# Performance work log

Hardware: AMD Instinct MI355X
Metric: run time of the kernel (lower is better)

## Reference

```python
import jax, jax.numpy as jnp
import numpy as np

B = 16384          # scenes (batch_size)
K = 16             # vehicles per scene (1 hero + 15 neighbors)
IN_LEN = 16        # in_length
OUT_LEN = 25       # out_length
ALL_LEN = 41       # all_length
T_H = IN_LEN - 1
ENC = 64           # encoder_size
N = B * K
NN = B * (K - 1)


def setup_inputs() -> dict:
    key = jax.random.key(0)
    ks = jax.random.split(key, 20)
    scene = jax.random.normal(ks[0], (N, 2, ALL_LEN), jnp.float32)
    idx = jnp.arange(N, dtype=jnp.int32)
    hero_index = idx[::K]                 # hero is first vehicle of each group
    nbr_index = idx[idx % K != 0]         # remaining K-1 vehicles, group-major
    w = lambda k, s: jax.random.normal(k, s, jnp.float32) * 0.1
    return {
        'scene': scene, 'hero_index': hero_index, 'nbr_index': nbr_index,
        'W_h1': w(ks[1], (2 * IN_LEN, 32)), 'b_h1': w(ks[2], (32,)),
        'W_h2': w(ks[3], (32, ENC)), 'b_h2': w(ks[4], (ENC,)),
        'W_f1': w(ks[5], (2 * OUT_LEN, 32)), 'b_f1': w(ks[6], (32,)),
        'W_f2': w(ks[7], (32, ENC)), 'b_f2': w(ks[8], (ENC,)),
        'W_dyn': w(ks[9], (ENC, 32)), 'b_dyn': w(ks[10], (32,)),
        'W_nbr': w(ks[11], (2 * IN_LEN, ENC)), 'b_nbr': w(ks[12], (ENC,)),
        'W_out': w(ks[13], (96, 128)), 'b_out': w(ks[14], (128,)),
        'W_op': w(ks[15], (128, 1)), 'b_op': w(ks[16], (1,)),
    }


def reference(scene, hero_index, nbr_index,
              W_h1, b_h1, W_h2, b_h2, W_f1, b_f1, W_f2, b_f2,
              W_dyn, b_dyn, W_nbr, b_nbr, W_out, b_out, W_op, b_op):
    lrelu = lambda x: jax.nn.leaky_relu(x, 0.1)
    # per-scene reference pose = hero position at t_h, broadcast to all vehicles
    ref = scene[hero_index, :, T_H][:, :, None]              # (B,2,1)
    scene = scene - jnp.repeat(ref, K, axis=0)               # (N,2,ALL_LEN)
    # per-scene, per-channel scale = max |history| over vehicles and time
    scale = jnp.abs(scene[:, :, :IN_LEN]).reshape(B, K, 2, IN_LEN).max(axis=(1, 3))  # (B,2)
    scene = scene / jnp.repeat(scale, K, axis=0)[:, :, None]
    hero = scene[hero_index]                                 # (B,2,ALL_LEN)
    nbrs = scene[nbr_index]                                  # (NN,2,ALL_LEN)
    hist = hero[:, :, :IN_LEN].transpose(0, 2, 1)            # (B,IN_LEN,2)
    fut = hero[:, :, IN_LEN:IN_LEN + OUT_LEN].transpose(0, 2, 1)  # (B,OUT_LEN,2)
    nb_hist = nbrs[:, :, :IN_LEN].transpose(0, 2, 1)         # (NN,IN_LEN,2)
    rel = jnp.repeat(hist, K - 1, axis=0) - nb_hist          # (NN,IN_LEN,2)
    hist_f = hist.reshape(B, 2 * IN_LEN)
    fut_f = fut.reshape(B, 2 * OUT_LEN)
    rel_f = rel.reshape(NN, 2 * IN_LEN)
    # hero history encoder (mlp_net) + dyn_emb
    hist_enc = lrelu(lrelu(hist_f @ W_h1 + b_h1) @ W_h2 + b_h2)
    hist_enc = lrelu(hist_enc @ W_dyn + b_dyn)
    # neighbor relative encoder + per-scene max pool + dyn_emb
    rela_enc = lrelu(rel_f @ W_nbr + b_nbr)                  # (NN,ENC)
    pooled = rela_enc.reshape(B, K - 1, ENC).max(axis=1)     # (B,ENC)
    pooled = lrelu(pooled @ W_dyn + b_dyn)
    # future encoder (mlp_net_fut) + dyn_emb
    fut_enc = lrelu(lrelu(fut_f @ W_f1 + b_f1) @ W_f2 + b_f2)
    fut_enc = lrelu(fut_enc @ W_dyn + b_dyn)
    enc = jnp.concatenate([hist_enc, pooled, fut_enc], axis=1)  # (B,96)
    feature_enc = lrelu(enc @ W_out + b_out)                 # (B,128)
    logit = jax.nn.sigmoid(feature_enc @ W_op + b_op)        # (B,1)
    return logit, feature_enc
```

## Files before the change

kernel.cpp:

```cpp
#include <hip/hip_runtime.h>
#include <math.h>

#define NB 16384

typedef short short8 __attribute__((ext_vector_type(8)));
typedef float f32x4 __attribute__((ext_vector_type(4)));

__device__ __forceinline__ float lrelu(float x){ return x > 0.f ? x : 0.1f*x; }

__device__ __forceinline__ unsigned short f2b(float f){
  unsigned u = __builtin_bit_cast(unsigned, f);
  u = (u + 0x7fffu + ((u >> 16) & 1u)) >> 16;
  return (unsigned short)u;
}

__device__ __forceinline__ short8 afrag(const unsigned short* tile, int stride_us, int kbase){
  const int l = threadIdx.x & 63;
  return *(const short8*)(tile + (size_t)(l & 15) * stride_us + kbase + ((l >> 4) * 8));
}

__device__ __forceinline__ short8 wfragT(const float* __restrict__ W, int ldn,
                                         int nbase, int kbase, int K){
  const int l = threadIdx.x & 63;
  const int n = nbase + (l & 15);
  const int k0 = kbase + ((l >> 4) * 8);
  short8 r;
  #pragma unroll
  for (int e = 0; e < 8; ++e){
    const int k = k0 + e;
    const float v = (k < K) ? W[k * ldn + n] : 0.f;
    r[e] = (short)f2b(v);
  }
  return r;
}

#define MFMA(a,b,c) __builtin_amdgcn_mfma_f32_16x16x32_bf16((a),(b),(c),0,0,0)

__global__ __launch_bounds__(512) void highway_fused(
    const float* __restrict__ scene,
    const float* __restrict__ W_h1, const float* __restrict__ b_h1,
    const float* __restrict__ W_h2, const float* __restrict__ b_h2,
    const float* __restrict__ W_f1, const float* __restrict__ b_f1,
    const float* __restrict__ W_f2, const float* __restrict__ b_f2,
    const float* __restrict__ W_dyn, const float* __restrict__ b_dyn,
    const float* __restrict__ W_nbr, const float* __restrict__ b_nbr,
    const float* __restrict__ W_out, const float* __restrict__ b_out,
    const float* __restrict__ W_op, const float* __restrict__ b_op,
    float* __restrict__ logit, float* __restrict__ feat)
{
  __shared__ __align__(16) unsigned short An[15][16][40];
  __shared__ __align__(16) unsigned short Ah[16][40];
  __shared__ __align__(16) unsigned short Af[16][72];
  __shared__ __align__(16) unsigned short Apool[16][72];
  __shared__ __align__(16) unsigned short As1h[16][40];
  __shared__ __align__(16) unsigned short As1f[16][40];
  __shared__ __align__(16) unsigned short As2h[16][72];
  __shared__ __align__(16) unsigned short As2f[16][72];
  __shared__ __align__(16) unsigned short Aenc[16][104];
  __shared__ float tmpP[4][16][16];
  __shared__ float red[8][16];

  const int tid = threadIdx.x;
  const int w = tid >> 6, l = tid & 63;
  const int g = tid >> 5;
  const int s = tid & 31;
  const int c = s >> 4, t = s & 15;
  const int g0 = blockIdx.x * 16;
  const float* sc = scene + (size_t)(g0 + g) * 1312;

  const short8 wn  = wfragT(W_nbr, 64, (w & 3) * 16, 0, 32);
  const short8 s1a = (w < 2) ? wfragT(W_h1, 32, (w & 1) * 16, 0, 32)
                             : wfragT(W_f1, 32, (w & 1) * 16, 0, 50);
  const short8 s1b = wfragT(W_f1, 32, (w & 1) * 16, 32, 50);
  const short8 wd0 = wfragT(W_dyn, 32, (w & 1) * 16, 0, 64);
  const short8 wd1 = wfragT(W_dyn, 32, (w & 1) * 16, 32, 64);
  const short8 s2  = (w < 4) ? wfragT(W_h2, 64, w * 16, 0, 32)
                             : wfragT(W_f2, 64, (w & 3) * 16, 0, 32);
  const short8 wo0 = wfragT(W_out, 128, w * 16, 0, 96);
  const short8 wo1 = wfragT(W_out, 128, w * 16, 32, 96);
  const short8 wo2 = wfragT(W_out, 128, w * 16, 64, 96);
  const float  wop = W_op[w * 16 + (l & 15)];

  float v[16];
  #pragma unroll
  for (int k = 0; k < 16; ++k) v[k] = sc[k * 82 + c * 41 + t];
  const float vf0 = sc[c * 41 + 16 + t];
  const float vf1 = (t < 9) ? sc[c * 41 + 32 + t] : 0.f;

  const float ref = __shfl(v[0], (l & 32) | (c << 4) | 15, 64);
  float m = 0.f;
  #pragma unroll
  for (int k = 0; k < 16; ++k) m = fmaxf(m, fabsf(v[k] - ref));
  m = fmaxf(m, __shfl_xor(m, 1, 64));
  m = fmaxf(m, __shfl_xor(m, 2, 64));
  m = fmaxf(m, __shfl_xor(m, 4, 64));
  m = fmaxf(m, __shfl_xor(m, 8, 64));
  const float inv = 1.f / m;

  Ah[g][2 * t + c] = f2b((v[0] - ref) * inv);
  #pragma unroll
  for (int j = 0; j < 15; ++j)
    An[j][g][2 * t + c] = f2b((v[0] - v[j + 1]) * inv);
  Af[g][2 * t + c] = f2b((vf0 - ref) * inv);
  Af[g][2 * t + 32 + c] = (t < 9) ? f2b((vf1 - ref) * inv) : (unsigned short)0;

  __syncthreads();

  {
    const int nt = w & 3;
    const int jbase = (w >> 2) * 8;
    const int njt = (w >> 2) ? 7 : 8;
    const float bn = b_nbr[nt * 16 + (l & 15)];
    f32x4 pm = {-1e30f, -1e30f, -1e30f, -1e30f};
    for (int jj = 0; jj < njt; ++jj){
      const short8 a = afrag(&An[jbase + jj][0][0], 40, 0);
      f32x4 acc = {0.f, 0.f, 0.f, 0.f};
      acc = MFMA(a, wn, acc);
      #pragma unroll
      for (int r = 0; r < 4; ++r) pm[r] = fmaxf(pm[r], lrelu(acc[r] + bn));
    }
    if (w >= 4){
      #pragma unroll
      for (int r = 0; r < 4; ++r) tmpP[nt][(l >> 4) * 4 + r][l & 15] = pm[r];
    }
    __syncthreads();
    if (w < 4){
      #pragma unroll
      for (int r = 0; r < 4; ++r){
        const float q = fmaxf(pm[r], tmpP[nt][(l >> 4) * 4 + r][l & 15]);
        Apool[(l >> 4) * 4 + r][nt * 16 + (l & 15)] = f2b(q);
      }
    }
  }
  __syncthreads();

  if (w < 2){
    const short8 a = afrag(&Ah[0][0], 40, 0);
    f32x4 acc = {0.f, 0.f, 0.f, 0.f};
    acc = MFMA(a, s1a, acc);
    const float bb = b_h1[(w & 1) * 16 + (l & 15)];
    #pragma unroll
    for (int r = 0; r < 4; ++r)
      As1h[(l >> 4) * 4 + r][(w & 1) * 16 + (l & 15)] = f2b(lrelu(acc[r] + bb));
  } else if (w < 4){
    const short8 a0 = afrag(&Af[0][0], 72, 0);
    const short8 a1 = afrag(&Af[0][0], 72, 32);
    f32x4 acc = {0.f, 0.f, 0.f, 0.f};
    acc = MFMA(a0, s1a, acc);
    acc = MFMA(a1, s1b, acc);
    const float bb = b_f1[(w & 1) * 16 + (l & 15)];
    #pragma unroll
    for (int r = 0; r < 4; ++r)
      As1f[(l >> 4) * 4 + r][(w & 1) * 16 + (l & 15)] = f2b(lrelu(acc[r] + bb));
  } else if (w < 6){
    const short8 a0 = afrag(&Apool[0][0], 72, 0);
    const short8 a1 = afrag(&Apool[0][0], 72, 32);
    f32x4 acc = {0.f, 0.f, 0.f, 0.f};
    acc = MFMA(a0, wd0, acc);
    acc = MFMA(a1, wd1, acc);
    const float bb = b_dyn[(w & 1) * 16 + (l & 15)];
    #pragma unroll
    for (int r = 0; r < 4; ++r)
      Aenc[(l >> 4) * 4 + r][32 + (w & 1) * 16 + (l & 15)] = f2b(lrelu(acc[r] + bb));
  }
  __syncthreads();

  if (w < 4){
    const short8 a = afrag(&As1h[0][0], 40, 0);
    f32x4 acc = {0.f, 0.f, 0.f, 0.f};
    acc = MFMA(a, s2, acc);
    const float bb = b_h2[w * 16 + (l & 15)];
    #pragma unroll
    for (int r = 0; r < 4; ++r)
      As2h[(l >> 4) * 4 + r][w * 16 + (l & 15)] = f2b(lrelu(acc[r] + bb));
  } else {
    const short8 a = afrag(&As1f[0][0], 40, 0);
    f32x4 acc = {0.f, 0.f, 0.f, 0.f};
    acc = MFMA(a, s2, acc);
    const float bb = b_f2[(w & 3) * 16 + (l & 15)];
    #pragma unroll
    for (int r = 0; r < 4; ++r)
      As2f[(l >> 4) * 4 + r][(w & 3) * 16 + (l & 15)] = f2b(lrelu(acc[r] + bb));
  }
  __syncthreads();

  if (w < 2){
    const short8 a0 = afrag(&As2h[0][0], 72, 0);
    const short8 a1 = afrag(&As2h[0][0], 72, 32);
    f32x4 acc = {0.f, 0.f, 0.f, 0.f};
    acc = MFMA(a0, wd0, acc);
    acc = MFMA(a1, wd1, acc);
    const float bb = b_dyn[(w & 1) * 16 + (l & 15)];
    #pragma unroll
    for (int r = 0; r < 4; ++r)
      Aenc[(l >> 4) * 4 + r][(w & 1) * 16 + (l & 15)] = f2b(lrelu(acc[r] + bb));
  } else if (w < 4){
    const short8 a0 = afrag(&As2f[0][0], 72, 0);
    const short8 a1 = afrag(&As2f[0][0], 72, 32);
    f32x4 acc = {0.f, 0.f, 0.f, 0.f};
    acc = MFMA(a0, wd0, acc);
    acc = MFMA(a1, wd1, acc);
    const float bb = b_dyn[(w & 1) * 16 + (l & 15)];
    #pragma unroll
    for (int r = 0; r < 4; ++r)
      Aenc[(l >> 4) * 4 + r][64 + (w & 1) * 16 + (l & 15)] = f2b(lrelu(acc[r] + bb));
  }
  __syncthreads();

  {
    const short8 a0 = afrag(&Aenc[0][0], 104, 0);
    const short8 a1 = afrag(&Aenc[0][0], 104, 32);
    const short8 a2 = afrag(&Aenc[0][0], 104, 64);
    f32x4 acc = {0.f, 0.f, 0.f, 0.f};
    acc = MFMA(a0, wo0, acc);
    acc = MFMA(a1, wo1, acc);
    acc = MFMA(a2, wo2, acc);
    const float bb = b_out[w * 16 + (l & 15)];
    float p[4];
    #pragma unroll
    for (int r = 0; r < 4; ++r){
      const int gg = (l >> 4) * 4 + r;
      const float fe = lrelu(acc[r] + bb);
      feat[(size_t)(g0 + gg) * 128 + w * 16 + (l & 15)] = fe;
      p[r] = fe * wop;
    }
    #pragma unroll
    for (int r = 0; r < 4; ++r){
      p[r] += __shfl_xor(p[r], 1, 64);
      p[r] += __shfl_xor(p[r], 2, 64);
      p[r] += __shfl_xor(p[r], 4, 64);
      p[r] += __shfl_xor(p[r], 8, 64);
    }
    if ((l & 15) == 0){
      #pragma unroll
      for (int r = 0; r < 4; ++r) red[w][(l >> 4) * 4 + r] = p[r];
    }
  }
  __syncthreads();

  if (tid < 16){
    float sacc = b_op[0];
    #pragma unroll
    for (int ww = 0; ww < 8; ++ww) sacc += red[ww][tid];
    logit[g0 + tid] = 1.f / (1.f + expf(-sacc));
  }
}

extern "C" void kernel_launch(void* const* d_in, const int* in_sizes, int n_in,
                              void* d_out, int out_size, void* d_ws, size_t ws_size,
                              hipStream_t stream)
{
  (void)in_sizes; (void)n_in; (void)out_size; (void)d_ws; (void)ws_size;
  const float* scene = (const float*)d_in[0];
  const float* W_h1  = (const float*)d_in[3];
  const float* b_h1  = (const float*)d_in[4];
  const float* W_h2  = (const float*)d_in[5];
  const float* b_h2  = (const float*)d_in[6];
  const float* W_f1  = (const float*)d_in[7];
  const float* b_f1  = (const float*)d_in[8];
  const float* W_f2  = (const float*)d_in[9];
  const float* b_f2  = (const float*)d_in[10];
  const float* W_dyn = (const float*)d_in[11];
  const float* b_dyn = (const float*)d_in[12];
  const float* W_nbr = (const float*)d_in[13];
  const float* b_nbr = (const float*)d_in[14];
  const float* W_out = (const float*)d_in[15];
  const float* b_out = (const float*)d_in[16];
  const float* W_op  = (const float*)d_in[17];
  const float* b_op  = (const float*)d_in[18];

  float* logit = (float*)d_out;
  float* feat  = logit + NB;

  highway_fused<<<NB / 16, 512, 0, stream>>>(scene,
      W_h1, b_h1, W_h2, b_h2, W_f1, b_f1, W_f2, b_f2, W_dyn, b_dyn,
      W_nbr, b_nbr, W_out, b_out, W_op, b_op, logit, feat);
}
```

Baseline: 27.81 us.

## Precompute bf16 weight fragments in prep kernel and vectorize scene loads

Adds a small prep kernel that converts all weight matrices into bf16 MFMA fragment layout in workspace, so each block loads fragments with single 16-byte loads when needed instead of doing strided scalar fp32 gathers and conversions up front. The scene load is restructured so each thread reads one vehicle-channel row with float4 loads and writes packed short8 rows to shared memory, with the hero row broadcast by shuffles. Feature pairing is permuted to match (channel-major k ordering absorbed into the weight fragments), the max-pool scratch is stored as bf16, and launch bounds hint higher occupancy. It adds a second kernel launch and relies on the workspace buffer.

New measurement: 57.00 us. 105% more time.

```diff
diff --git a/kernel.cpp b/kernel.cpp
--- a/kernel.cpp
+++ b/kernel.cpp
@@ -1,4 +1,5 @@
 #include <hip/hip_runtime.h>
+#include <hip/hip_bf16.h>
 #include <math.h>
 
 #define NB 16384
@@ -13,39 +14,74 @@
   u = (u + 0x7fffu + ((u >> 16) & 1u)) >> 16;
   return (unsigned short)u;
 }
+__device__ __forceinline__ float b2f(unsigned short u){
+  unsigned x = (unsigned)u << 16;
+  return __builtin_bit_cast(float, x);
+}
+
+#define MFMA(a,b,c) __builtin_amdgcn_mfma_f32_16x16x32_bf16((a),(b),(c),0,0,0)
 
 __device__ __forceinline__ short8 afrag(const unsigned short* tile, int stride_us, int kbase){
   const int l = threadIdx.x & 63;
   return *(const short8*)(tile + (size_t)(l & 15) * stride_us + kbase + ((l >> 4) * 8));
 }
 
-__device__ __forceinline__ short8 wfragT(const float* __restrict__ W, int ldn,
-                                         int nbase, int kbase, int K){
-  const int l = threadIdx.x & 63;
-  const int n = nbase + (l & 15);
-  const int k0 = kbase + ((l >> 4) * 8);
-  short8 r;
+__device__ __forceinline__ short8 ldfrag(const unsigned short* __restrict__ frags, int slot, int w){
+  return *(const short8*)(frags + ((size_t)((slot * 8 + w) * 64 + (threadIdx.x & 63)) * 8));
+}
+
+__global__ __launch_bounds__(64) void prep_frags(
+    const float* __restrict__ W_h1, const float* __restrict__ W_f1,
+    const float* __restrict__ W_h2, const float* __restrict__ W_f2,
+    const float* __restrict__ W_dyn, const float* __restrict__ W_nbr,
+    const float* __restrict__ W_out, unsigned short* __restrict__ frags)
+{
+  const int bid = blockIdx.x;
+  const int slot = bid >> 3, w = bid & 7;
+  const int l = threadIdx.x;
+  const int n16 = l & 15, q = l >> 4;
+  short8 r = {0,0,0,0,0,0,0,0};
   #pragma unroll
   for (int e = 0; e < 8; ++e){
-    const int k = k0 + e;
-    const float v = (k < K) ? W[k * ldn + n] : 0.f;
+    const int p = q * 8 + e;
+    int i = -1, n = -1, ldn = 0;
+    const float* W = nullptr;
+    switch (slot){
+      case 0: W = W_nbr; ldn = 64; n = (w & 3) * 16 + n16;
+              i = 2 * (p & 15) + (p >> 4); break;
+      case 1:
+        if (w < 2){ W = W_h1; ldn = 32; n = (w & 1) * 16 + n16;
+                    i = 2 * (p & 15) + (p >> 4); }
+        else if (w < 4){ W = W_f1; ldn = 32; n = (w & 1) * 16 + n16;
+                    i = (p < 25) ? 2 * p : -1; }
+        break;
+      case 2:
+        if (w >= 2 && w < 4){ W = W_f1; ldn = 32; n = (w & 1) * 16 + n16;
+                    i = (p < 25) ? 2 * p + 1 : -1; }
+        break;
+      case 3: W = W_dyn; ldn = 32; n = (w & 1) * 16 + n16; i = p;      break;
+      case 4: W = W_dyn; ldn = 32; n = (w & 1) * 16 + n16; i = 32 + p; break;
+      case 5: if (w < 4){ W = W_h2; ldn = 64; n = w * 16 + n16; }
+              else      { W = W_f2; ldn = 64; n = (w & 3) * 16 + n16; }
+              i = p; break;
+      case 6: W = W_out; ldn = 128; n = w * 16 + n16; i = p;      break;
+      case 7: W = W_out; ldn = 128; n = w * 16 + n16; i = 32 + p; break;
+      case 8: W = W_out; ldn = 128; n = w * 16 + n16; i = 64 + p; break;
+    }
+    const float v = (W && i >= 0) ? W[i * ldn + n] : 0.f;
     r[e] = (short)f2b(v);
   }
-  return r;
-}
-
-#define MFMA(a,b,c) __builtin_amdgcn_mfma_f32_16x16x32_bf16((a),(b),(c),0,0,0)
-
-__global__ __launch_bounds__(512) void highway_fused(
+  *(short8*)(frags + (size_t)(bid * 64 + l) * 8) = r;
+}
+
+__global__ __launch_bounds__(512, 4) void highway_fused(
     const float* __restrict__ scene,
-    const float* __restrict__ W_h1, const float* __restrict__ b_h1,
-    const float* __restrict__ W_h2, const float* __restrict__ b_h2,
-    const float* __restrict__ W_f1, const float* __restrict__ b_f1,
-    const float* __restrict__ W_f2, const float* __restrict__ b_f2,
-    const float* __restrict__ W_dyn, const float* __restrict__ b_dyn,
-    const float* __restrict__ W_nbr, const float* __restrict__ b_nbr,
-    const float* __restrict__ W_out, const float* __restrict__ b_out,
-    const float* __restrict__ W_op, const float* __restrict__ b_op,
+    const unsigned short* __restrict__ frags,
+    const float* __restrict__ b_h1, const float* __restrict__ b_h2,
+    const float* __restrict__ b_f1, const float* __restrict__ b_f2,
+    const float* __restrict__ b_dyn, const float* __restrict__ b_nbr,
+    const float* __restrict__ b_out, const float* __restrict__ W_op,
+    const float* __restrict__ b_op,
     float* __restrict__ logit, float* __restrict__ feat)
 {
   __shared__ __align__(16) unsigned short An[15][16][40];
@@ -57,171 +93,224 @@
   __shared__ __align__(16) unsigned short As2h[16][72];
   __shared__ __align__(16) unsigned short As2f[16][72];
   __shared__ __align__(16) unsigned short Aenc[16][104];
-  __shared__ float tmpP[4][16][16];
+  __shared__ unsigned short tmpP[4][16][16];
   __shared__ float red[8][16];
 
   const int tid = threadIdx.x;
   const int w = tid >> 6, l = tid & 63;
-  const int g = tid >> 5;
-  const int s = tid & 31;
-  const int c = s >> 4, t = s & 15;
   const int g0 = blockIdx.x * 16;
-  const float* sc = scene + (size_t)(g0 + g) * 1312;
-
-  const short8 wn  = wfragT(W_nbr, 64, (w & 3) * 16, 0, 32);
-  const short8 s1a = (w < 2) ? wfragT(W_h1, 32, (w & 1) * 16, 0, 32)
-                             : wfragT(W_f1, 32, (w & 1) * 16, 0, 50);
-  const short8 s1b = wfragT(W_f1, 32, (w & 1) * 16, 32, 50);
-  const short8 wd0 = wfragT(W_dyn, 32, (w & 1) * 16, 0, 64);
-  const short8 wd1 = wfragT(W_dyn, 32, (w & 1) * 16, 32, 64);
-  const short8 s2  = (w < 4) ? wfragT(W_h2, 64, w * 16, 0, 32)
-                             : wfragT(W_f2, 64, (w & 3) * 16, 0, 32);
-  const short8 wo0 = wfragT(W_out, 128, w * 16, 0, 96);
-  const short8 wo1 = wfragT(W_out, 128, w * 16, 32, 96);
-  const short8 wo2 = wfragT(W_out, 128, w * 16, 64, 96);
-  const float  wop = W_op[w * 16 + (l & 15)];
-
-  float v[16];
-  #pragma unroll
-  for (int k = 0; k < 16; ++k) v[k] = sc[k * 82 + c * 41 + t];
-  const float vf0 = sc[c * 41 + 16 + t];
-  const float vf1 = (t < 9) ? sc[c * 41 + 32 + t] : 0.f;
-
-  const float ref = __shfl(v[0], (l & 32) | (c << 4) | 15, 64);
-  float m = 0.f;
-  #pragma unroll
-  for (int k = 0; k < 16; ++k) m = fmaxf(m, fabsf(v[k] - ref));
-  m = fmaxf(m, __shfl_xor(m, 1, 64));
-  m = fmaxf(m, __shfl_xor(m, 2, 64));
-  m = fmaxf(m, __shfl_xor(m, 4, 64));
-  m = fmaxf(m, __shfl_xor(m, 8, 64));
-  const float inv = 1.f / m;
-
-  Ah[g][2 * t + c] = f2b((v[0] - ref) * inv);
-  #pragma unroll
-  for (int j = 0; j < 15; ++j)
-    An[j][g][2 * t + c] = f2b((v[0] - v[j + 1]) * inv);
-  Af[g][2 * t + c] = f2b((vf0 - ref) * inv);
-  Af[g][2 * t + 32 + c] = (t < 9) ? f2b((vf1 - ref) * inv) : (unsigned short)0;
-
-  __syncthreads();
 
   {
+    const int g = tid >> 5, s = tid & 31;
+    const int k = s >> 1, c = s & 1;
+    const float* sc = scene + (size_t)(g0 + g) * 1312;
+
+    const int idx0 = k * 82 + c * 41;
+    const int ab = idx0 & ~3;
+    const int off = idx0 & 3;
+    float wb[20];
+    {
+      const float4* p4 = (const float4*)(sc + ab);
+      #pragma unroll
+      for (int q = 0; q < 5; ++q){
+        const float4 t4 = p4[q];
+        wb[4*q] = t4.x; wb[4*q+1] = t4.y; wb[4*q+2] = t4.z; wb[4*q+3] = t4.w;
+      }
+    }
+    const bool hi2 = (off & 2) != 0, hi1 = (off & 1) != 0;
+    float u[17];
+    #pragma unroll
+    for (int t = 0; t < 17; ++t) u[t] = hi2 ? wb[t+2] : wb[t];
+    float v[16];
+    #pragma unroll
+    for (int t = 0; t < 16; ++t) v[t] = hi1 ? u[t+1] : u[t];
+
+    float h[16];
+    const int hsrc = (l & 32) | c;
+    #pragma unroll
+    for (int t = 0; t < 16; ++t) h[t] = __shfl(v[t], hsrc, 64);
+    const float ref = h[15];
+
+    float m = 0.f;
+    #pragma unroll
+    for (int t = 0; t < 16; ++t) m = fmaxf(m, fabsf(v[t] - ref));
+    m = fmaxf(m, __shfl_xor(m, 2, 64));
+    m = fmaxf(m, __shfl_xor(m, 4, 64));
+    m = fmaxf(m, __shfl_xor(m, 8, 64));
+    m = fmaxf(m, __shfl_xor(m, 16, 64));
+    const float inv = 1.f / m;
+
+    if (k == 0){
+      short8 r0, r1;
+      #pragma unroll
+      for (int t = 0; t < 8; ++t){
+        r0[t] = (short)f2b((v[t] - ref) * inv);
+        r1[t] = (short)f2b((v[t+8] - ref) * inv);
+      }
+      *(short8*)&Ah[g][c*16]   = r0;
+      *(short8*)&Ah[g][c*16+8] = r1;
+      const int fab = (c * 41 + 16) & ~3;
+      float fb[28];
+      const float4* f4 = (const float4*)(sc + fab);
+      #pragma unroll
+      for (int q = 0; q < 7; ++q){
+        const float4 t4 = f4[q];
+        fb[4*q]=t4.x; fb[4*q+1]=t4.y; fb[4*q+2]=t4.z; fb[4*q+3]=t4.w;
+      }
+      short8 q0,q1,q2,q3;
+      #pragma unroll
+      for (int t = 0; t < 8; ++t){
+        const float a0 = c ? fb[t+1]  : fb[t];
+        const float a1 = c ? fb[t+9]  : fb[t+8];
+        const float a2 = c ? fb[t+17] : fb[t+16];
+        q0[t] = (short)f2b((a0 - ref) * inv);
+        q1[t] = (short)f2b((a1 - ref) * inv);
+        q2[t] = (short)f2b((a2 - ref) * inv);
+        if (t == 0){
+          const float a3 = c ? fb[25] : fb[24];
+          q3[t] = (short)f2b((a3 - ref) * inv);
+        } else q3[t] = 0;
+      }
+      *(short8*)&Af[g][c*32]    = q0;
+      *(short8*)&Af[g][c*32+8]  = q1;
+      *(short8*)&Af[g][c*32+16] = q2;
+      *(short8*)&Af[g][c*32+24] = q3;
+    } else {
+      short8 r0, r1;
+      #pragma unroll
+      for (int t = 0; t < 8; ++t){
+        r0[t] = (short)f2b((h[t]   - v[t])   * inv);
+        r1[t] = (short)f2b((h[t+8] - v[t+8]) * inv);
+      }
+      *(short8*)&An[k-1][g][c*16]   = r0;
+      *(short8*)&An[k-1][g][c*16+8] = r1;
+    }
+  }
+  __syncthreads();
+
+  {
+    const short8 wn = ldfrag(frags, 0, w);
     const int nt = w & 3;
     const int jbase = (w >> 2) * 8;
     const int njt = (w >> 2) ? 7 : 8;
     const float bn = b_nbr[nt * 16 + (l & 15)];
-    f32x4 pm = {-1e30f, -1e30f, -1e30f, -1e30f};
+    f32x4 pm = {-1e30f,-1e30f,-1e30f,-1e30f};
     for (int jj = 0; jj < njt; ++jj){
       const short8 a = afrag(&An[jbase + jj][0][0], 40, 0);
-      f32x4 acc = {0.f, 0.f, 0.f, 0.f};
+      f32x4 acc = {0.f,0.f,0.f,0.f};
       acc = MFMA(a, wn, acc);
       #pragma unroll
       for (int r = 0; r < 4; ++r) pm[r] = fmaxf(pm[r], lrelu(acc[r] + bn));
     }
     if (w >= 4){
       #pragma unroll
-      for (int r = 0; r < 4; ++r) tmpP[nt][(l >> 4) * 4 + r][l & 15] = pm[r];
+      for (int r = 0; r < 4; ++r) tmpP[nt][(l>>4)*4+r][l&15] = f2b(pm[r]);
     }
     __syncthreads();
     if (w < 4){
       #pragma unroll
       for (int r = 0; r < 4; ++r){
-        const float q = fmaxf(pm[r], tmpP[nt][(l >> 4) * 4 + r][l & 15]);
-        Apool[(l >> 4) * 4 + r][nt * 16 + (l & 15)] = f2b(q);
+        const float q = fmaxf(pm[r], b2f(tmpP[nt][(l>>4)*4+r][l&15]));
+        Apool[(l>>4)*4+r][nt*16+(l&15)] = f2b(q);
       }
     }
   }
   __syncthreads();
 
   if (w < 2){
+    const short8 s1 = ldfrag(frags, 1, w);
     const short8 a = afrag(&Ah[0][0], 40, 0);
-    f32x4 acc = {0.f, 0.f, 0.f, 0.f};
-    acc = MFMA(a, s1a, acc);
-    const float bb = b_h1[(w & 1) * 16 + (l & 15)];
+    f32x4 acc = {0.f,0.f,0.f,0.f};
+    acc = MFMA(a, s1, acc);
+    const float bb = b_h1[(w&1)*16 + (l&15)];
     #pragma unroll
     for (int r = 0; r < 4; ++r)
-      As1h[(l >> 4) * 4 + r][(w & 1) * 16 + (l & 15)] = f2b(lrelu(acc[r] + bb));
+      As1h[(l>>4)*4+r][(w&1)*16+(l&15)] = f2b(lrelu(acc[r] + bb));
   } else if (w < 4){
+    const short8 s1  = ldfrag(frags, 1, w);
+    const short8 s1x = ldfrag(frags, 2, w);
     const short8 a0 = afrag(&Af[0][0], 72, 0);
     const short8 a1 = afrag(&Af[0][0], 72, 32);
-    f32x4 acc = {0.f, 0.f, 0.f, 0.f};
-    acc = MFMA(a0, s1a, acc);
-    acc = MFMA(a1, s1b, acc);
-    const float bb = b_f1[(w & 1) * 16 + (l & 15)];
+    f32x4 acc = {0.f,0.f,0.f,0.f};
+    acc = MFMA(a0, s1, acc);
+    acc = MFMA(a1, s1x, acc);
+    const float bb = b_f1[(w&1)*16 + (l&15)];
     #pragma unroll
     for (int r = 0; r < 4; ++r)
-      As1f[(l >> 4) * 4 + r][(w & 1) * 16 + (l & 15)] = f2b(lrelu(acc[r] + bb));
+      As1f[(l>>4)*4+r][(w&1)*16+(l&15)] = f2b(lrelu(acc[r] + bb));
   } else if (w < 6){
+    const short8 d0 = ldfrag(frags, 3, w);
+    const short8 d1 = ldfrag(frags, 4, w);
     const short8 a0 = afrag(&Apool[0][0], 72, 0);
     const short8 a1 = afrag(&Apool[0][0], 72, 32);
-    f32x4 acc = {0.f, 0.f, 0.f, 0.f};
-    acc = MFMA(a0, wd0, acc);
-    acc = MFMA(a1, wd1, acc);
-    const float bb = b_dyn[(w & 1) * 16 + (l & 15)];
+    f32x4 acc = {0.f,0.f,0.f,0.f};
+    acc = MFMA(a0, d0, acc);
+    acc = MFMA(a1, d1, acc);
+    const float bb = b_dyn[(w&1)*16 + (l&15)];
     #pragma unroll
     for (int r = 0; r < 4; ++r)
-      Aenc[(l >> 4) * 4 + r][32 + (w & 1) * 16 + (l & 15)] = f2b(lrelu(acc[r] + bb));
+      Aenc[(l>>4)*4+r][32+(w&1)*16+(l&15)] = f2b(lrelu(acc[r] + bb));
+  }
+  __syncthreads();
+
+  {
+    const short8 s2 = ldfrag(frags, 5, w);
+    if (w < 4){
+      const short8 a = afrag(&As1h[0][0], 40, 0);
+      f32x4 acc = {0.f,0.f,0.f,0.f};
+      acc = MFMA(a, s2, acc);
+      const float bb = b_h2[w*16 + (l&15)];
+      #pragma unroll
+      for (int r = 0; r < 4; ++r)
+        As2h[(l>>4)*4+r][w*16+(l&15)] = f2b(lrelu(acc[r] + bb));
+    } else {
+      const short8 a = afrag(&As1f[0][0], 40, 0);
+      f32x4 acc = {0.f,0.f,0.f,0.f};
+      acc = MFMA(a, s2, acc);
+      const float bb = b_f2[(w&3)*16 + (l&15)];
+      #pragma unroll
+      for (int r = 0; r < 4; ++r)
+        As2f[(l>>4)*4+r][(w&3)*16+(l&15)] = f2b(lrelu(acc[r] + bb));
+    }
   }
   __syncthreads();
 
   if (w < 4){
-    const short8 a = afrag(&As1h[0][0], 40, 0);
-    f32x4 acc = {0.f, 0.f, 0.f, 0.f};
-    acc = MFMA(a, s2, acc);
-    const float bb = b_h2[w * 16 + (l & 15)];
+    const short8 d0 = ldfrag(frags, 3, w);
+    const short8 d1 = ldfrag(frags, 4, w);
+    const unsigned short* src = (w < 2) ? &As2h[0][0] : &As2f[0][0];
+    const short8 a0 = afrag(src, 72, 0);
+    const short8 a1 = afrag(src, 72, 32);
+    f32x4 acc = {0.f,0.f,0.f,0.f};
+    acc = MFMA(a0, d0, acc);
+    acc = MFMA(a1, d1, acc);
+    const float bb = b_dyn[(w&1)*16 + (l&15)];
+    const int base = (w < 2) ? 0 : 64;
     #pragma unroll
     for (int r = 0; r < 4; ++r)
-      As2h[(l >> 4) * 4 + r][w * 16 + (l & 15)] = f2b(lrelu(acc[r] + bb));
-  } else {
-    const short8 a = afrag(&As1f[0][0], 40, 0);
-    f32x4 acc = {0.f, 0.f, 0.f, 0.f};
-    acc = MFMA(a, s2, acc);
-    const float bb = b_f2[(w & 3) * 16 + (l & 15)];
-    #pragma unroll
-    for (int r = 0; r < 4; ++r)
-      As2f[(l >> 4) * 4 + r][(w & 3) * 16 + (l & 15)] = f2b(lrelu(acc[r] + bb));
-  }
-  __syncthreads();
-
-  if (w < 2){
-    const short8 a0 = afrag(&As2h[0][0], 72, 0);
-    const short8 a1 = afrag(&As2h[0][0], 72, 32);
-    f32x4 acc = {0.f, 0.f, 0.f, 0.f};
-    acc = MFMA(a0, wd0, acc);
-    acc = MFMA(a1, wd1, acc);
-    const float bb = b_dyn[(w & 1) * 16 + (l & 15)];
-    #pragma unroll
-    for (int r = 0; r < 4; ++r)
-      Aenc[(l >> 4) * 4 + r][(w & 1) * 16 + (l & 15)] = f2b(lrelu(acc[r] + bb));
-  } else if (w < 4){
-    const short8 a0 = afrag(&As2f[0][0], 72, 0);
-    const short8 a1 = afrag(&As2f[0][0], 72, 32);
-    f32x4 acc = {0.f, 0.f, 0.f, 0.f};
-    acc = MFMA(a0, wd0, acc);
-    acc = MFMA(a1, wd1, acc);
-    const float bb = b_dyn[(w & 1) * 16 + (l & 15)];
-    #pragma unroll
-    for (int r = 0; r < 4; ++r)
-      Aenc[(l >> 4) * 4 + r][64 + (w & 1) * 16 + (l & 15)] = f2b(lrelu(acc[r] + bb));
+      Aenc[(l>>4)*4+r][base+(w&1)*16+(l&15)] = f2b(lrelu(acc[r] + bb));
   }
   __syncthreads();
 
   {
+    const short8 wo0 = ldfrag(frags, 6, w);
+    const short8 wo1 = ldfrag(frags, 7, w);
+    const short8 wo2 = ldfrag(frags, 8, w);
     const short8 a0 = afrag(&Aenc[0][0], 104, 0);
     const short8 a1 = afrag(&Aenc[0][0], 104, 32);
     const short8 a2 = afrag(&Aenc[0][0], 104, 64);
-    f32x4 acc = {0.f, 0.f, 0.f, 0.f};
+    f32x4 acc = {0.f,0.f,0.f,0.f};
     acc = MFMA(a0, wo0, acc);
     acc = MFMA(a1, wo1, acc);
     acc = MFMA(a2, wo2, acc);
-    const float bb = b_out[w * 16 + (l & 15)];
+    const float bb = b_out[w*16 + (l&15)];
+    const float wop = W_op[w*16 + (l&15)];
     float p[4];
     #pragma unroll
     for (int r = 0; r < 4; ++r){
-      const int gg = (l >> 4) * 4 + r;
+      const int gg = (l>>4)*4 + r;
       const float fe = lrelu(acc[r] + bb);
-      feat[(size_t)(g0 + gg) * 128 + w * 16 + (l & 15)] = fe;
+      feat[(size_t)(g0 + gg) * 128 + w*16 + (l&15)] = fe;
       p[r] = fe * wop;
     }
     #pragma unroll
@@ -233,7 +322,7 @@
     }
     if ((l & 15) == 0){
       #pragma unroll
-      for (int r = 0; r < 4; ++r) red[w][(l >> 4) * 4 + r] = p[r];
+      for (int r = 0; r < 4; ++r) red[w][(l>>4)*4 + r] = p[r];
     }
   }
   __syncthreads();
@@ -250,7 +339,7 @@
                               void* d_out, int out_size, void* d_ws, size_t ws_size,
                               hipStream_t stream)
 {
-  (void)in_sizes; (void)n_in; (void)out_size; (void)d_ws; (void)ws_size;
+  (void)in_sizes; (void)n_in; (void)out_size; (void)ws_size;
   const float* scene = (const float*)d_in[0];
   const float* W_h1  = (const float*)d_in[3];
   const float* b_h1  = (const float*)d_in[4];
@@ -269,10 +358,12 @@
   const float* W_op  = (const float*)d_in[17];
   const float* b_op  = (const float*)d_in[18];
 
+  unsigned short* frags = (unsigned short*)d_ws;
+
   float* logit = (float*)d_out;
   float* feat  = logit + NB;
 
-  highway_fused<<<NB / 16, 512, 0, stream>>>(scene,
-      W_h1, b_h1, W_h2, b_h2, W_f1, b_f1, W_f2, b_f2, W_dyn, b_dyn,
-      W_nbr, b_nbr, W_out, b_out, W_op, b_op, logit, feat);
-}
+  prep_frags<<<72, 64, 0, stream>>>(W_h1, W_f1, W_h2, W_f2, W_dyn, W_nbr, W_out, frags);
+  highway_fused<<<NB / 16, 512, 0, stream>>>(scene, frags,
+      b_h1, b_h2, b_f1, b_f2, b_dyn, b_nbr, b_out, W_op, b_op, logit, feat);
+}
```
